# Optimization experiments

Measured on AMD Instinct MI355X. Metric: run time of the kernel, lower is better.

The kernel has to match this reference:

```python
import jax, jax.numpy as jnp
import numpy as np

N = 2097152
D = 128
CLASSES = 1000


def setup_inputs() -> dict:
    key = jax.random.key(0)
    k1, k2 = jax.random.split(key)
    X = jax.random.normal(k1, (N, D), dtype=jnp.float32)
    labels = jax.random.randint(k2, (N,), 0, CLASSES, dtype=jnp.int64)
    return {"X": X, "labels": labels, "classes": CLASSES}


def reference(X, labels, classes):
    # DistributionTracker.forward: per-label scatter-add of
    #   count (num), sum(X) (miu accumulator), sum(X^2) (std accumulator)
    # Fused here as three segment_sums over the label axis.
    num = jax.ops.segment_sum(jnp.ones((X.shape[0],), dtype=X.dtype), labels,
                              num_segments=classes)          # (c,)
    miu = jax.ops.segment_sum(X, labels, num_segments=classes)       # (c, D)
    sqr = jax.ops.segment_sum(X * X, labels, num_segments=classes)   # (c, D)
    # Pack into a single (c, 1 + 2D) array: [num | sum(X) | sum(X^2)]
    return jnp.concatenate([num[:, None], miu, sqr], axis=1)
```

## Files before the change

### kernel.cpp

```cpp
#include <hip/hip_runtime.h>


constexpr int DIM    = 128;
constexpr int ROWLEN = 2 * DIM + 1;

constexpr int HIST_B = 256;
constexpr int HIST_T = 256;

__global__ __launch_bounds__(HIST_T)
void hist_kernel(const int* __restrict__ labels, int N, int classes,
                 unsigned* __restrict__ hist_part,
                 float* __restrict__ out, int out_total)
{
    for (int i = blockIdx.x * HIST_T + threadIdx.x; i < out_total;
         i += HIST_B * HIST_T) out[i] = 0.0f;

    __shared__ unsigned lh[1024];
    for (int i = threadIdx.x; i < 1024; i += HIST_T) lh[i] = 0;
    __syncthreads();

    const int gtid = blockIdx.x * HIST_T + threadIdx.x;
    const int gstr = HIST_B * HIST_T;
    const int N4   = N >> 2;
    const int4* l4 = (const int4*)labels;
    for (int i = gtid; i < N4; i += gstr) {
        const int4 v = l4[i];
        if ((unsigned)v.x < (unsigned)classes) atomicAdd(&lh[v.x], 1u);
        if ((unsigned)v.y < (unsigned)classes) atomicAdd(&lh[v.y], 1u);
        if ((unsigned)v.z < (unsigned)classes) atomicAdd(&lh[v.z], 1u);
        if ((unsigned)v.w < (unsigned)classes) atomicAdd(&lh[v.w], 1u);
    }
    for (int i = (N4 << 2) + gtid; i < N; i += gstr) {
        const unsigned l = (unsigned)labels[i];
        if (l < (unsigned)classes) atomicAdd(&lh[l], 1u);
    }
    __syncthreads();
    unsigned* hp = hist_part + (size_t)blockIdx.x * 1024;
    for (int i = threadIdx.x; i < 1024; i += HIST_T) hp[i] = lh[i];
}

__global__ __launch_bounds__(1024)
void prefix_kernel(const unsigned* __restrict__ hist_part,
                   unsigned* __restrict__ off,
                   unsigned* __restrict__ cursor, int classes)
{
    __shared__ unsigned s[1024];
    const int tid = threadIdx.x;
    unsigned a0 = 0, a1 = 0, a2 = 0, a3 = 0;
    for (int b = 0; b < HIST_B; b += 4) {
        a0 += hist_part[(b + 0) * 1024 + tid];
        a1 += hist_part[(b + 1) * 1024 + tid];
        a2 += hist_part[(b + 2) * 1024 + tid];
        a3 += hist_part[(b + 3) * 1024 + tid];
    }
    s[tid] = (tid < classes) ? (a0 + a1 + a2 + a3) : 0u;
    __syncthreads();
    for (int d = 1; d < 1024; d <<= 1) {
        unsigned v = (tid >= d) ? s[tid - d] : 0u;
        __syncthreads();
        s[tid] += v;
        __syncthreads();
    }
    if (tid == 0) { off[0] = 0; cursor[0] = 0; }
    if (tid < classes) {
        off[tid + 1] = s[tid];
        if (tid > 0) cursor[tid] = s[tid - 1];
    }
}

constexpr int SCAT_T  = 256;
constexpr int SCAT_IT = 16;

__global__ __launch_bounds__(SCAT_T)
void scatter_kernel(const int* __restrict__ labels, int N, int classes,
                    unsigned* __restrict__ cursor,
                    unsigned* __restrict__ idx)
{
    __shared__ unsigned lh[1024], lbase[1024];
    const int tid  = threadIdx.x;
    const int tile = blockIdx.x * (SCAT_T * SCAT_IT);
    for (int i = tid; i < 1024; i += SCAT_T) lh[i] = 0;
    __syncthreads();

    int lab[SCAT_IT];
#pragma unroll
    for (int k = 0; k < SCAT_IT; ++k) {
        const int row = tile + k * SCAT_T + tid;
        lab[k] = -1;
        if (row < N) {
            const unsigned l = (unsigned)labels[row];
            if (l < (unsigned)classes) { lab[k] = (int)l; atomicAdd(&lh[l], 1u); }
        }
    }
    __syncthreads();
    for (int c = tid; c < classes; c += SCAT_T) {
        if (lh[c]) lbase[c] = atomicAdd(&cursor[c], lh[c]);
        lh[c] = 0;
    }
    __syncthreads();
#pragma unroll
    for (int k = 0; k < SCAT_IT; ++k) {
        if (lab[k] >= 0) {
            const unsigned l   = (unsigned)lab[k];
            const unsigned row = (unsigned)(tile + k * SCAT_T + tid);
            idx[lbase[l] + atomicAdd(&lh[l], 1u)] = row;
        }
    }
}

constexpr int SPLIT = 4;
constexpr int U     = 8;

__global__ __launch_bounds__(64)
void accum_kernel(const float* __restrict__ X,
                  const unsigned* __restrict__ gidx,
                  const unsigned* __restrict__ off,
                  float* __restrict__ out)
{
    const int c = blockIdx.x / SPLIT;
    const int h = blockIdx.x % SPLIT;
    const unsigned s   = off[c];
    const unsigned cnt = off[c + 1] - s;
    if (cnt == 0) return;
    const unsigned s_h = s + (unsigned)(((unsigned long long)cnt * h) / SPLIT);
    const unsigned e_h = s + (unsigned)(((unsigned long long)cnt * (h + 1)) / SPLIT);
    if (s_h >= e_h) return;

    const int lane = threadIdx.x;

    float2 m[U], q[U];
#pragma unroll
    for (int u = 0; u < U; ++u) {
        m[u].x = m[u].y = 0.0f; q[u].x = q[u].y = 0.0f;
    }

    unsigned p = s_h;
    for (; p + U <= e_h; p += U) {
        const float2* Xr[U];
#pragma unroll
        for (int u = 0; u < U; ++u) {
            const unsigned r = __builtin_amdgcn_readfirstlane(gidx[p + u]);
            Xr[u] = (const float2*)(X + (size_t)r * DIM);
        }
#pragma unroll
        for (int u = 0; u < U; ++u) {
            const float2 x = Xr[u][lane];
            m[u].x += x.x;                   m[u].y += x.y;
            q[u].x = fmaf(x.x, x.x, q[u].x); q[u].y = fmaf(x.y, x.y, q[u].y);
        }
    }
    for (; p < e_h; ++p) {
        const unsigned r = __builtin_amdgcn_readfirstlane(gidx[p]);
        const float2 x = ((const float2*)(X + (size_t)r * DIM))[lane];
        m[0].x += x.x;                   m[0].y += x.y;
        q[0].x = fmaf(x.x, x.x, q[0].x); q[0].y = fmaf(x.y, x.y, q[0].y);
    }

#pragma unroll
    for (int u = 1; u < U; ++u) {
        m[0].x += m[u].x; m[0].y += m[u].y;
        q[0].x += q[u].x; q[0].y += q[u].y;
    }

    float* po = out + (size_t)c * ROWLEN;
    unsafeAtomicAdd(po + 1   + 2 * lane, m[0].x);
    unsafeAtomicAdd(po + 2   + 2 * lane, m[0].y);
    unsafeAtomicAdd(po + 129 + 2 * lane, q[0].x);
    unsafeAtomicAdd(po + 130 + 2 * lane, q[0].y);
    if (lane == 0) unsafeAtomicAdd(po, (float)(e_h - s_h));
}

constexpr int FB_T = 512;
constexpr int FB_W = FB_T / 64;
constexpr int FB_CG = 63;

__global__ __launch_bounds__(FB_T, 2)
void fb_kernel(const float* __restrict__ X, const int* __restrict__ labels,
               float* __restrict__ out, int N, int classes, int rpc)
{
    __shared__ float part[FB_CG * ROWLEN];
    const int tid = threadIdx.x, lane = tid & 63, wid = tid >> 6;
    const int gbase = blockIdx.y * FB_CG;
    for (int i = tid; i < FB_CG * ROWLEN; i += FB_T) part[i] = 0.0f;
    __syncthreads();
    const long long row0 = (long long)blockIdx.x * rpc;
    int rows = rpc;
    if (row0 + rows > N) rows = (int)((long long)N - row0);
    for (int base = wid * 64; base < rows; base += FB_W * 64) {
        const int nb = min(64, rows - base);
        int lab = -1;
        if (lane < nb) lab = labels[row0 + base + lane];
        const int lc = lab - gbase;
        const bool in = (lab >= 0) && (lc >= 0) && (lc < FB_CG) && (lab < classes);
        unsigned long long mask = __ballot(in);
        while (mask) {
            const int j = __ffsll((long long)mask) - 1;
            mask &= mask - 1;
            const int cc = __shfl(lc, j);
            const size_t ridx = (size_t)(row0 + base + j) * DIM;
            const float x0 = X[ridx + lane];
            const float x1 = X[ridx + lane + 64];
            float* pp = &part[cc * ROWLEN];
            unsafeAtomicAdd(&pp[1 + lane], x0);
            unsafeAtomicAdd(&pp[65 + lane], x1);
            unsafeAtomicAdd(&pp[129 + lane], x0 * x0);
            unsafeAtomicAdd(&pp[193 + lane], x1 * x1);
            if (lane == 0) unsafeAtomicAdd(&pp[0], 1.0f);
        }
    }
    __syncthreads();
    const int cmax = min(FB_CG, classes - gbase);
    float* gout = out + (size_t)gbase * ROWLEN;
    for (int i = tid; i < cmax * ROWLEN; i += FB_T) {
        const float vv = part[i];
        if (vv != 0.0f) unsafeAtomicAdd(&gout[i], vv);
    }
}

extern "C" void kernel_launch(void* const* d_in, const int* in_sizes, int n_in,
                              void* d_out, int out_size, void* d_ws, size_t ws_size,
                              hipStream_t stream)
{
    const float* X      = (const float*)d_in[0];
    const int*   labels = (const int*)d_in[1];
    float*       out    = (float*)d_out;

    const int N       = in_sizes[1];
    const int classes = out_size / ROWLEN;

    const size_t HP_BYTES = (size_t)HIST_B * 1024 * 4;
    const size_t need = HP_BYTES + 16384 + (size_t)N * 4;
    const bool fast = (ws_size >= need) && (classes <= 1024);

    if (fast) {
        unsigned* hist_part = (unsigned*)d_ws;
        unsigned* off    = (unsigned*)((char*)d_ws + HP_BYTES);
        unsigned* cursor = (unsigned*)((char*)d_ws + HP_BYTES + 8192);
        unsigned* idx    = (unsigned*)((char*)d_ws + HP_BYTES + 16384);

        hist_kernel<<<HIST_B, HIST_T, 0, stream>>>(labels, N, classes,
                                                   hist_part, out, out_size);
        prefix_kernel<<<1, 1024, 0, stream>>>(hist_part, off, cursor, classes);
        const int sblocks = (N + SCAT_T * SCAT_IT - 1) / (SCAT_T * SCAT_IT);
        scatter_kernel<<<sblocks, SCAT_T, 0, stream>>>(labels, N, classes,
                                                       cursor, idx);
        accum_kernel<<<classes * SPLIT, 64, 0, stream>>>(X, idx, off, out);
    } else {
        hipMemsetAsync(d_out, 0, (size_t)out_size * sizeof(float), stream);
        const int groups = (classes + FB_CG - 1) / FB_CG;
        const int target_chunks = 32;
        int rpc = (N + target_chunks - 1) / target_chunks;
        const int batch = FB_W * 64;
        rpc = ((rpc + batch - 1) / batch) * batch;
        const int chunks = (N + rpc - 1) / rpc;
        dim3 grid(chunks, groups);
        fb_kernel<<<grid, FB_T, 0, stream>>>(X, labels, out, N, classes, rpc);
    }
}
```

Baseline: 245.5 us.

## Parallelize histogram column reduction and prefetch row indices in accumulation

The per-block histograms are now stored transposed (class-major), so a new multi-block colsum kernel reduces each class's 256 partial counts with one wavefront and a shuffle reduction. The single-block prefix kernel then reads only the 1024 final counts instead of looping over the whole partial-histogram buffer. Separately, the accumulation loop loads the next group of sorted row indices one iteration ahead, so index loads overlap the X row loads. This costs an extra kernel launch and a little register pressure from the prefetch buffer.

```diff
diff --git a/kernel.cpp b/kernel.cpp
--- a/kernel.cpp
+++ b/kernel.cpp
@@ -35,25 +35,33 @@
         if (l < (unsigned)classes) atomicAdd(&lh[l], 1u);
     }
     __syncthreads();
-    unsigned* hp = hist_part + (size_t)blockIdx.x * 1024;
-    for (int i = threadIdx.x; i < 1024; i += HIST_T) hp[i] = lh[i];
+    for (int i = threadIdx.x; i < 1024; i += HIST_T)
+        hist_part[(size_t)i * HIST_B + blockIdx.x] = lh[i];
+}
+
+__global__ __launch_bounds__(256)
+void colsum_kernel(const unsigned* __restrict__ hist_part,
+                   unsigned* __restrict__ hist)
+{
+    const int wid  = threadIdx.x >> 6;
+    const int lane = threadIdx.x & 63;
+    const int c    = blockIdx.x * 4 + wid;
+    const uint4* hp4 = (const uint4*)(hist_part + (size_t)c * HIST_B);
+    const uint4 v = hp4[lane];
+    unsigned s = v.x + v.y + v.z + v.w;
+#pragma unroll
+    for (int d = 32; d; d >>= 1) s += __shfl_xor(s, d);
+    if (lane == 0) hist[c] = s;
 }
 
 __global__ __launch_bounds__(1024)
-void prefix_kernel(const unsigned* __restrict__ hist_part,
+void prefix_kernel(const unsigned* __restrict__ hist,
                    unsigned* __restrict__ off,
                    unsigned* __restrict__ cursor, int classes)
 {
     __shared__ unsigned s[1024];
     const int tid = threadIdx.x;
-    unsigned a0 = 0, a1 = 0, a2 = 0, a3 = 0;
-    for (int b = 0; b < HIST_B; b += 4) {
-        a0 += hist_part[(b + 0) * 1024 + tid];
-        a1 += hist_part[(b + 1) * 1024 + tid];
-        a2 += hist_part[(b + 2) * 1024 + tid];
-        a3 += hist_part[(b + 3) * 1024 + tid];
-    }
-    s[tid] = (tid < classes) ? (a0 + a1 + a2 + a3) : 0u;
+    s[tid] = (tid < classes) ? hist[tid] : 0u;
     __syncthreads();
     for (int d = 1; d < 1024; d <<= 1) {
         unsigned v = (tid >= d) ? s[tid - d] : 0u;
@@ -135,16 +143,23 @@
     }
 
     unsigned p = s_h;
+    unsigned nxt[U];
+    if (p + U <= e_h) {
+#pragma unroll
+        for (int u = 0; u < U; ++u) nxt[u] = gidx[p + u];
+    }
     for (; p + U <= e_h; p += U) {
-        const float2* Xr[U];
+        unsigned cur[U];
+#pragma unroll
+        for (int u = 0; u < U; ++u) cur[u] = nxt[u];
+        if (p + 2 * U <= e_h) {
+#pragma unroll
+            for (int u = 0; u < U; ++u) nxt[u] = gidx[p + U + u];
+        }
 #pragma unroll
         for (int u = 0; u < U; ++u) {
-            const unsigned r = __builtin_amdgcn_readfirstlane(gidx[p + u]);
-            Xr[u] = (const float2*)(X + (size_t)r * DIM);
-        }
-#pragma unroll
-        for (int u = 0; u < U; ++u) {
-            const float2 x = Xr[u][lane];
+            const unsigned r = __builtin_amdgcn_readfirstlane(cur[u]);
+            const float2 x = ((const float2*)(X + (size_t)r * DIM))[lane];
             m[u].x += x.x;                   m[u].y += x.y;
             q[u].x = fmaf(x.x, x.x, q[u].x); q[u].y = fmaf(x.y, x.y, q[u].y);
         }
@@ -228,19 +243,21 @@
     const int N       = in_sizes[1];
     const int classes = out_size / ROWLEN;
 
-    const size_t HP_BYTES = (size_t)HIST_B * 1024 * 4;
+    const size_t HP_BYTES = (size_t)1024 * HIST_B * 4;
     const size_t need = HP_BYTES + 16384 + (size_t)N * 4;
     const bool fast = (ws_size >= need) && (classes <= 1024);
 
     if (fast) {
         unsigned* hist_part = (unsigned*)d_ws;
-        unsigned* off    = (unsigned*)((char*)d_ws + HP_BYTES);
-        unsigned* cursor = (unsigned*)((char*)d_ws + HP_BYTES + 8192);
+        unsigned* hist   = (unsigned*)((char*)d_ws + HP_BYTES);
+        unsigned* off    = (unsigned*)((char*)d_ws + HP_BYTES + 4096);
+        unsigned* cursor = (unsigned*)((char*)d_ws + HP_BYTES + 12288);
         unsigned* idx    = (unsigned*)((char*)d_ws + HP_BYTES + 16384);
 
         hist_kernel<<<HIST_B, HIST_T, 0, stream>>>(labels, N, classes,
                                                    hist_part, out, out_size);
-        prefix_kernel<<<1, 1024, 0, stream>>>(hist_part, off, cursor, classes);
+        colsum_kernel<<<256, 256, 0, stream>>>(hist_part, hist);
+        prefix_kernel<<<1, 1024, 0, stream>>>(hist, off, cursor, classes);
         const int sblocks = (N + SCAT_T * SCAT_IT - 1) / (SCAT_T * SCAT_IT);
         scatter_kernel<<<sblocks, SCAT_T, 0, stream>>>(labels, N, classes,
                                                        cursor, idx);
```

New measurement: 247.5 us. About the same (+0.8%).

## Reduce per-class accumulation in shared memory and drop output zeroing and atomics

Applied to the files above, without the earlier changes.

The accumulation kernel now uses one block per class with eight wavefronts, each summing a slice of the class's rows. The partial sums are combined through shared memory and written with plain stores instead of global atomics. Because every output element is now written directly, the histogram kernel no longer zeroes the output buffer. The cost is a block-level barrier, and each class gets eight waves instead of four.

```diff
diff --git a/kernel.cpp b/kernel.cpp
--- a/kernel.cpp
+++ b/kernel.cpp
@@ -9,12 +9,8 @@
 
 __global__ __launch_bounds__(HIST_T)
 void hist_kernel(const int* __restrict__ labels, int N, int classes,
-                 unsigned* __restrict__ hist_part,
-                 float* __restrict__ out, int out_total)
-{
-    for (int i = blockIdx.x * HIST_T + threadIdx.x; i < out_total;
-         i += HIST_B * HIST_T) out[i] = 0.0f;
-
+                 unsigned* __restrict__ hist_part)
+{
     __shared__ unsigned lh[1024];
     for (int i = threadIdx.x; i < 1024; i += HIST_T) lh[i] = 0;
     __syncthreads();
@@ -108,25 +104,26 @@
     }
 }
 
-constexpr int SPLIT = 4;
+constexpr int SPLIT = 8;
+constexpr int AT    = 64 * SPLIT;
 constexpr int U     = 8;
 
-__global__ __launch_bounds__(64)
+__global__ __launch_bounds__(AT, 8)
 void accum_kernel(const float* __restrict__ X,
                   const unsigned* __restrict__ gidx,
                   const unsigned* __restrict__ off,
                   float* __restrict__ out)
 {
-    const int c = blockIdx.x / SPLIT;
-    const int h = blockIdx.x % SPLIT;
+    const int c = blockIdx.x;
     const unsigned s   = off[c];
     const unsigned cnt = off[c + 1] - s;
-    if (cnt == 0) return;
-    const unsigned s_h = s + (unsigned)(((unsigned long long)cnt * h) / SPLIT);
-    const unsigned e_h = s + (unsigned)(((unsigned long long)cnt * (h + 1)) / SPLIT);
-    if (s_h >= e_h) return;
-
-    const int lane = threadIdx.x;
+
+    const int tid  = threadIdx.x;
+    const int lane = tid & 63;
+    const int wid  = tid >> 6;
+
+    const unsigned s_h = s + (unsigned)(((unsigned long long)cnt * wid) / SPLIT);
+    const unsigned e_h = s + (unsigned)(((unsigned long long)cnt * (wid + 1)) / SPLIT);
 
     float2 m[U], q[U];
 #pragma unroll
@@ -162,12 +159,33 @@
         q[0].x += q[u].x; q[0].y += q[u].y;
     }
 
+    __shared__ float2 red_m[SPLIT][64];
+    __shared__ float2 red_q[SPLIT][64];
+    red_m[wid][lane] = m[0];
+    red_q[wid][lane] = q[0];
+    __syncthreads();
+
     float* po = out + (size_t)c * ROWLEN;
-    unsafeAtomicAdd(po + 1   + 2 * lane, m[0].x);
-    unsafeAtomicAdd(po + 2   + 2 * lane, m[0].y);
-    unsafeAtomicAdd(po + 129 + 2 * lane, q[0].x);
-    unsafeAtomicAdd(po + 130 + 2 * lane, q[0].y);
-    if (lane == 0) unsafeAtomicAdd(po, (float)(e_h - s_h));
+    if (tid < 64) {
+        float2 a = {0.0f, 0.0f};
+#pragma unroll
+        for (int w = 0; w < SPLIT; ++w) {
+            a.x += red_m[w][tid].x; a.y += red_m[w][tid].y;
+        }
+        po[1 + 2 * tid] = a.x;
+        po[2 + 2 * tid] = a.y;
+    } else if (tid < 128) {
+        const int l = tid - 64;
+        float2 a = {0.0f, 0.0f};
+#pragma unroll
+        for (int w = 0; w < SPLIT; ++w) {
+            a.x += red_q[w][l].x; a.y += red_q[w][l].y;
+        }
+        po[129 + 2 * l] = a.x;
+        po[130 + 2 * l] = a.y;
+    } else if (tid == 128) {
+        po[0] = (float)cnt;
+    }
 }
 
 constexpr int FB_T = 512;
@@ -239,12 +257,12 @@
         unsigned* idx    = (unsigned*)((char*)d_ws + HP_BYTES + 16384);
 
         hist_kernel<<<HIST_B, HIST_T, 0, stream>>>(labels, N, classes,
-                                                   hist_part, out, out_size);
+                                                   hist_part);
         prefix_kernel<<<1, 1024, 0, stream>>>(hist_part, off, cursor, classes);
         const int sblocks = (N + SCAT_T * SCAT_IT - 1) / (SCAT_T * SCAT_IT);
         scatter_kernel<<<sblocks, SCAT_T, 0, stream>>>(labels, N, classes,
                                                        cursor, idx);
-        accum_kernel<<<classes * SPLIT, 64, 0, stream>>>(X, idx, off, out);
+        accum_kernel<<<classes, AT, 0, stream>>>(X, idx, off, out);
     } else {
         hipMemsetAsync(d_out, 0, (size_t)out_size * sizeof(float), stream);
         const int groups = (classes + FB_CG - 1) / FB_CG;
```

After: 253.4 us. +3.2%, slower.
